# Optimization experiments

Measured on AMD Instinct MI355X. Metric: run time of the kernel, lower is better.

## Reference

```python
import jax, jax.numpy as jnp
import numpy as np

N_NODES = 100000
N_EDGES = 1600000
N_GRAPHS = 64
FEAT = 64
EMB = 64
HID = 64
VOCAB = 32


def setup_inputs() -> dict:
    key = jax.random.key(0)
    ks = jax.random.split(key, 20)
    w = lambda k, sh: (jax.random.normal(k, sh, jnp.float32) * 0.05)
    x = jax.random.normal(ks[0], (N_NODES, FEAT), jnp.float32)
    edge_index = jax.random.randint(ks[1], (2, N_EDGES), 0, N_NODES, dtype=jnp.int32).astype(jnp.int64)
    batch = jnp.sort(jax.random.randint(ks[2], (N_NODES,), 0, N_GRAPHS, dtype=jnp.int32)).astype(jnp.int64)
    return {
        'x': x, 'edge_index': edge_index, 'batch': batch,
        # RGCN layer 1 (single relation): relation weight, root weight, bias
        'W1': w(ks[3], (FEAT, EMB)), 'root1': w(ks[4], (FEAT, EMB)), 'b1': w(ks[5], (EMB,)),
        # RGCN layer 2
        'W2': w(ks[6], (EMB, HID)), 'root2': w(ks[7], (EMB, HID)), 'b2': w(ks[8], (HID,)),
        # init_h / init_c linear heads
        'Wh': w(ks[9], (HID, HID)), 'bh': w(ks[10], (HID,)),
        'Wc': w(ks[11], (HID, HID)), 'bc': w(ks[12], (HID,)),
        # output layer
        'Wo': w(ks[13], (HID, VOCAB)), 'bo': w(ks[14], (VOCAB,)),
    }


def _rgcn(x, edge_index, W, root, b):
    # PyG RGCNConv with num_relations=1, aggr='mean':
    # out[i] = mean_{j in N(i)} (x[j] @ W) + x[i] @ root + b
    src, dst = edge_index[0], edge_index[1]
    msg = x[src] @ W                                    # [E, out] gather + small GEMM
    agg = jax.ops.segment_sum(msg, dst, num_segments=x.shape[0])
    cnt = jax.ops.segment_sum(jnp.ones((edge_index.shape[1],), x.dtype), dst, num_segments=x.shape[0])
    agg = agg / jnp.maximum(cnt, 1.0)[:, None]
    return agg + x @ root + b


def reference(x, edge_index, batch, W1, root1, b1, W2, root2, b2, Wh, bh, Wc, bc, Wo, bo):
    h = jax.nn.relu(_rgcn(x, edge_index, W1, root1, b1))
    h = jax.nn.relu(_rgcn(h, edge_index, W2, root2, b2))
    # global_mean_pool over graph-assignment vector `batch`
    summ = jax.ops.segment_sum(h, batch, num_segments=N_GRAPHS)
    cnt = jax.ops.segment_sum(jnp.ones((h.shape[0],), h.dtype), batch, num_segments=N_GRAPHS)
    pooled = summ / jnp.maximum(cnt, 1.0)[:, None]      # [G, HID]
    hidden = pooled @ Wh + bh
    cell = pooled @ Wc + bc
    logits = jax.nn.log_softmax(hidden @ Wo + bo, axis=1)
    return (logits, hidden, cell)
```

## Files before the change

kernel.cpp:

```cpp
#include <hip/hip_runtime.h>
#include <hip/hip_bf16.h>


typedef __attribute__((ext_vector_type(8))) short short8;
typedef __attribute__((ext_vector_type(4))) float f32x4;
typedef __attribute__((ext_vector_type(2))) float f32x2;

#define RB 9
#define MAXBINS 256
#define CAP 12288
#define BCAP 14336
#define CHUNK 8192

__device__ inline float bf2f(unsigned short h) {
    return __uint_as_float(((unsigned int)h) << 16);
}
__device__ inline float bflo(unsigned int u) { return __uint_as_float(u << 16); }
__device__ inline float bfhi(unsigned int u) { return __uint_as_float(u & 0xffff0000u); }
__device__ inline unsigned short f2bf(float f) {
    unsigned int u = __float_as_uint(f);
    u = (u + 0x7fffu + ((u >> 16) & 1u)) >> 16;
    return (unsigned short)u;
}

__device__ inline void build_bfrag(const float* __restrict__ W,
                                   const float* __restrict__ R,
                                   int q, int mm, short8 bfrag[8][2]) {
#pragma unroll
    for (int t = 0; t < 8; ++t) {
        const int n = t * 16 + mm;
        const float* P = (n < 64) ? (W + n) : (R + n - 64);
#pragma unroll
        for (int c = 0; c < 2; ++c) {
#pragma unroll
            for (int j = 0; j < 8; ++j) {
                const int k = c * 32 + q * 8 + j;
                bfrag[t][c][j] = (short)f2bf(P[k * 64]);
            }
        }
    }
}

__device__ inline void store_xw_fp8(unsigned char* __restrict__ xw8, int rowbase, int q,
                                    int t, int mm, const f32x4& accT, int N) {
#pragma unroll
    for (int r = 0; r < 4; ++r) {
        const float v0 = accT[r];
        const float v1 = __shfl_down(v0, 1);
        const float v2 = __shfl_down(v0, 2);
        const float v3 = __shfl_down(v0, 3);
        const int orow = rowbase + q * 4 + r;
        if (!(mm & 3) && orow < N) {
            unsigned int u = (unsigned int)__builtin_amdgcn_cvt_pk_fp8_f32(v0, v1, 0, false);
            u = (unsigned int)__builtin_amdgcn_cvt_pk_fp8_f32(v2, v3, (int)u, true);
            *(unsigned int*)&xw8[(size_t)orow * 64 + t * 16 + mm] = u;
        }
    }
}

__global__ __launch_bounds__(256) void bin_gemm1(const int* __restrict__ src,
                                                 const int* __restrict__ dst,
                                                 unsigned int* __restrict__ coarse,
                                                 int* __restrict__ gcur,
                                                 int E, int BINS, int nbBin,
                                                 const float* __restrict__ x,
                                                 const float* __restrict__ W1,
                                                 const float* __restrict__ R1,
                                                 const float* __restrict__ bias,
                                                 unsigned char* __restrict__ xw8,
                                                 unsigned short* __restrict__ xrb,
                                                 int N) {
    __shared__ int cnt[MAXBINS];
    __shared__ int incl[MAXBINS];
    __shared__ int bstart[MAXBINS];
    __shared__ int bcur[MAXBINS];
    __shared__ int gbase[MAXBINS];
    __shared__ unsigned int stage[CHUNK];
    __shared__ unsigned char binOf[CHUNK];

    const int tid = threadIdx.x;
    if (blockIdx.x >= (unsigned)nbBin) {
        const int gb = blockIdx.x - nbBin;
        if (gb == 0 && tid < 16)
            *(unsigned int*)&xw8[(size_t)N * 64 + tid * 4] = 0u;

        const int lane = tid & 63;
        const int q = lane >> 4;
        const int mm = lane & 15;

        short8 bfrag[8][2];
        build_bfrag(W1, R1, q, mm, bfrag);
        float bv[4];
#pragma unroll
        for (int tt = 0; tt < 4; ++tt) bv[tt] = bias[tt * 16 + mm];

        const int wid = tid >> 6;
        const int gw = gb * 4 + wid;
        const int nw = 1024 * 4;
        const int ntiles = N >> 4;

        for (int tile = gw; tile < ntiles; tile += nw) {
            const int row0 = tile << 4;
            const float* ap = &x[(size_t)(row0 + mm) * 64 + q * 8];
            const float4 f0 = *(const float4*)ap;
            const float4 f1 = *(const float4*)(ap + 4);
            const float4 f2 = *(const float4*)(ap + 32);
            const float4 f3 = *(const float4*)(ap + 36);
            short8 a0, a1;
            a0[0] = (short)f2bf(f0.x); a0[1] = (short)f2bf(f0.y);
            a0[2] = (short)f2bf(f0.z); a0[3] = (short)f2bf(f0.w);
            a0[4] = (short)f2bf(f1.x); a0[5] = (short)f2bf(f1.y);
            a0[6] = (short)f2bf(f1.z); a0[7] = (short)f2bf(f1.w);
            a1[0] = (short)f2bf(f2.x); a1[1] = (short)f2bf(f2.y);
            a1[2] = (short)f2bf(f2.z); a1[3] = (short)f2bf(f2.w);
            a1[4] = (short)f2bf(f3.x); a1[5] = (short)f2bf(f3.y);
            a1[6] = (short)f2bf(f3.z); a1[7] = (short)f2bf(f3.w);
            f32x4 acc[8];
#pragma unroll
            for (int t = 0; t < 8; ++t) {
                acc[t] = (f32x4){0.f, 0.f, 0.f, 0.f};
                acc[t] = __builtin_amdgcn_mfma_f32_16x16x32_bf16(a0, bfrag[t][0], acc[t], 0, 0, 0);
                acc[t] = __builtin_amdgcn_mfma_f32_16x16x32_bf16(a1, bfrag[t][1], acc[t], 0, 0, 0);
            }
#pragma unroll
            for (int t = 0; t < 4; ++t) store_xw_fp8(xw8, row0, q, t, mm, acc[t], N);
#pragma unroll
            for (int t = 4; t < 8; ++t) {
#pragma unroll
                for (int r = 0; r < 4; ++r) {
                    const float v = acc[t][r] + bv[t - 4];
                    const float vn = __shfl_down(v, 1);
                    if (!(mm & 1)) {
                        const unsigned int u = (unsigned int)f2bf(v) | ((unsigned int)f2bf(vn) << 16);
                        *(unsigned int*)&xrb[(size_t)(row0 + q * 4 + r) * 64 + (t - 4) * 16 + mm] = u;
                    }
                }
            }
        }
        return;
    }

    const int chunk0 = blockIdx.x * CHUNK;
    int myS[32], myD[32];
#pragma unroll
    for (int k = 0; k < 32; ++k) {
        const int idx = chunk0 + k * 256 + tid;
        if (idx < E) { myS[k] = src[idx]; myD[k] = dst[idx]; }
        else myD[k] = -1;
    }
    cnt[tid] = 0;
    __syncthreads();
#pragma unroll
    for (int k = 0; k < 32; ++k)
        if (myD[k] >= 0) atomicAdd(&cnt[myD[k] >> RB], 1);
    __syncthreads();
    incl[tid] = cnt[tid];
    __syncthreads();
    for (int off = 1; off < 256; off <<= 1) {
        int t = (tid >= off) ? incl[tid - off] : 0;
        __syncthreads();
        incl[tid] += t;
        __syncthreads();
    }
    bstart[tid] = incl[tid] - cnt[tid];
    bcur[tid] = incl[tid] - cnt[tid];
    __syncthreads();
#pragma unroll
    for (int k = 0; k < 32; ++k) {
        if (myD[k] >= 0) {
            const int b = myD[k] >> RB;
            const int pos = atomicAdd(&bcur[b], 1);
            stage[pos] = (unsigned int)myS[k] | ((unsigned int)(myD[k] & ((1 << RB) - 1)) << 17);
            binOf[pos] = (unsigned char)b;
        }
    }
    __syncthreads();
    if (tid < BINS && cnt[tid] > 0)
        gbase[tid] = tid * CAP + atomicAdd(&gcur[tid], cnt[tid]);
    __syncthreads();
    int total = E - chunk0;
    if (total > CHUNK) total = CHUNK;
    for (int idx = tid; idx < total; idx += 256) {
        const int b = binOf[idx];
        coarse[gbase[b] + (idx - bstart[b])] = stage[idx];
    }
}

__global__ __launch_bounds__(256) void finalize_csr(const unsigned int* __restrict__ coarse,
                                                    const int* __restrict__ gcur,
                                                    int* __restrict__ bucket,
                                                    int* __restrict__ pstart,
                                                    int* __restrict__ degarr,
                                                    int N, int BINS) {
    __shared__ int ncnt[512];
    __shared__ int pexcl[512];
    __shared__ int ncur[512];
    __shared__ int s2[256];

    const int tid = threadIdx.x;
    const int b = blockIdx.x;
    const int cb = gcur[b];
    const int base = b * BCAP;
    const unsigned int* reg = coarse + (size_t)b * CAP;
    const int node0 = b << RB;
    int nloc = N - node0;
    if (nloc > 512) nloc = 512;

    ncnt[tid] = 0; ncnt[tid + 256] = 0;
    __syncthreads();
    for (int idx = tid; idx < cb; idx += 256)
        atomicAdd(&ncnt[reg[idx] >> 17], 1);
    __syncthreads();
    const int p0 = (ncnt[2 * tid] + 15) & ~15;
    const int p1 = (ncnt[2 * tid + 1] + 15) & ~15;
    s2[tid] = p0 + p1;
    __syncthreads();
    for (int off = 1; off < 256; off <<= 1) {
        int t = (tid >= off) ? s2[tid - off] : 0;
        __syncthreads();
        s2[tid] += t;
        __syncthreads();
    }
    const int pairExcl = s2[tid] - (p0 + p1);
    pexcl[2 * tid] = pairExcl;
    pexcl[2 * tid + 1] = pairExcl + p0;
    ncur[2 * tid] = pairExcl;
    ncur[2 * tid + 1] = pairExcl + p0;
    __syncthreads();
    for (int i = tid; i < nloc; i += 256) {
        pstart[node0 + i] = base + pexcl[i];
        degarr[node0 + i] = ncnt[i];
        const int dg = ncnt[i];
        const int pd = (dg + 15) & ~15;
        for (int j = dg; j < pd; ++j) bucket[base + pexcl[i] + j] = N;
    }
    for (int idx = tid; idx < cb; idx += 256) {
        const unsigned int e = reg[idx];
        const int p = atomicAdd(&ncur[e >> 17], 1);
        bucket[base + p] = (int)(e & 0x1FFFFu);
    }
}

__global__ __launch_bounds__(256) void aggregate(const unsigned char* __restrict__ xw8,
                                                 const unsigned short* __restrict__ xrb,
                                                 const int* __restrict__ pstart,
                                                 const int* __restrict__ degarr,
                                                 const int* __restrict__ bucket,
                                                 unsigned short* __restrict__ outb,
                                                 int N) {
    const int lane = threadIdx.x & 63;
    const int quarter = lane >> 4;
    const int fl = lane & 15;
    const int wid = threadIdx.x >> 6;
    const int gw = blockIdx.x * 4 + wid;
    const int nw = gridDim.x * 4;

    for (int i = gw; i < N; i += 4 * nw) {
        int idxs[4], r0[4], dg[4], pd[4];
#pragma unroll
        for (int j = 0; j < 4; ++j) {
            idxs[j] = i + j * nw;
            const bool hasJ = idxs[j] < N;
            const int ii = hasJ ? idxs[j] : i;
            r0[j] = pstart[ii];
            dg[j] = hasJ ? degarr[ii] : 0;
            pd[j] = (dg[j] + 15) & ~15;
        }
        int pdM = pd[0];
#pragma unroll
        for (int j = 1; j < 4; ++j) pdM = pd[j] > pdM ? pd[j] : pdM;

        float acc[4][4];
#pragma unroll
        for (int j = 0; j < 4; ++j)
#pragma unroll
            for (int c = 0; c < 4; ++c) acc[j][c] = 0.f;

        for (int base = 0; base < pdM; base += 64) {
            int s[4];
#pragma unroll
            for (int j = 0; j < 4; ++j) {
                const int rem = pd[j] - base;
                s[j] = (lane < rem) ? bucket[r0[j] + base + lane] : N;
            }
            int mx = pdM - base;
            if (mx > 64) mx = 64;
            for (int t = 0; t < mx; t += 16) {
                unsigned int u[4][4];
#pragma unroll
                for (int j = 0; j < 4; ++j)
#pragma unroll
                    for (int p = 0; p < 4; ++p) {
                        const int rr = __shfl(s[j], t + 4 * p + quarter);
                        u[j][p] = *(const unsigned int*)&xw8[(size_t)rr * 64 + fl * 4];
                    }
#pragma unroll
                for (int j = 0; j < 4; ++j)
#pragma unroll
                    for (int p = 0; p < 4; ++p) {
                        const f32x2 lo = __builtin_amdgcn_cvt_pk_f32_fp8(u[j][p], false);
                        const f32x2 hi = __builtin_amdgcn_cvt_pk_f32_fp8(u[j][p], true);
                        acc[j][0] += lo.x; acc[j][1] += lo.y;
                        acc[j][2] += hi.x; acc[j][3] += hi.y;
                    }
            }
        }
#pragma unroll
        for (int j = 0; j < 4; ++j)
#pragma unroll
            for (int c = 0; c < 4; ++c) {
                acc[j][c] += __shfl_xor(acc[j][c], 16);
                acc[j][c] += __shfl_xor(acc[j][c], 32);
            }

        if (quarter == 0) {
#pragma unroll
            for (int j = 0; j < 4; ++j) {
                if (idxs[j] < N) {
                    const float inv = 1.0f / (float)(dg[j] > 0 ? dg[j] : 1);
                    const uint2 ur = *(const uint2*)&xrb[(size_t)idxs[j] * 64 + fl * 4];
                    const float o0 = fmaxf(acc[j][0] * inv + bflo(ur.x), 0.f);
                    const float o1 = fmaxf(acc[j][1] * inv + bfhi(ur.x), 0.f);
                    const float o2 = fmaxf(acc[j][2] * inv + bflo(ur.y), 0.f);
                    const float o3 = fmaxf(acc[j][3] * inv + bfhi(ur.y), 0.f);
                    uint2 w;
                    w.x = (unsigned int)f2bf(o0) | ((unsigned int)f2bf(o1) << 16);
                    w.y = (unsigned int)f2bf(o2) | ((unsigned int)f2bf(o3) << 16);
                    *(uint2*)&outb[(size_t)idxs[j] * 64 + fl * 4] = w;
                }
            }
        }
    }
}

__global__ __launch_bounds__(256) void gemm_xwr2(const unsigned short* __restrict__ xin,
                                                 const float* __restrict__ W2,
                                                 const float* __restrict__ R2,
                                                 const float* __restrict__ bias,
                                                 unsigned char* __restrict__ xw8,
                                                 unsigned short* __restrict__ xrb,
                                                 int M) {
    if (blockIdx.x == 0 && threadIdx.x < 16)
        *(unsigned int*)&xw8[(size_t)M * 64 + threadIdx.x * 4] = 0u;

    const int lane = threadIdx.x & 63;
    const int q = lane >> 4;
    const int mm = lane & 15;

    short8 bfrag[8][2];
    build_bfrag(W2, R2, q, mm, bfrag);
    float bv[4];
#pragma unroll
    for (int tt = 0; tt < 4; ++tt) bv[tt] = bias[tt * 16 + mm];

    const int wid = threadIdx.x >> 6;
    const int gw = blockIdx.x * 4 + wid;
    const int nw = gridDim.x * 4;
    const int ntiles = M >> 4;

    for (int tile = gw; tile < ntiles; tile += nw) {
        const int row0 = tile << 4;
        const short8 a0 = *(const short8*)&xin[(size_t)(row0 + mm) * 64 + q * 8];
        const short8 a1 = *(const short8*)&xin[(size_t)(row0 + mm) * 64 + 32 + q * 8];
        f32x4 acc[8];
#pragma unroll
        for (int t = 0; t < 8; ++t) {
            acc[t] = (f32x4){0.f, 0.f, 0.f, 0.f};
            acc[t] = __builtin_amdgcn_mfma_f32_16x16x32_bf16(a0, bfrag[t][0], acc[t], 0, 0, 0);
            acc[t] = __builtin_amdgcn_mfma_f32_16x16x32_bf16(a1, bfrag[t][1], acc[t], 0, 0, 0);
        }
#pragma unroll
        for (int t = 0; t < 4; ++t) store_xw_fp8(xw8, row0, q, t, mm, acc[t], M);
#pragma unroll
        for (int t = 4; t < 8; ++t) {
#pragma unroll
            for (int r = 0; r < 4; ++r) {
                const float v = acc[t][r] + bv[t - 4];
                const float vn = __shfl_down(v, 1);
                if (!(mm & 1)) {
                    const unsigned int u = (unsigned int)f2bf(v) | ((unsigned int)f2bf(vn) << 16);
                    *(unsigned int*)&xrb[(size_t)(row0 + q * 4 + r) * 64 + (t - 4) * 16 + mm] = u;
                }
            }
        }
    }
}

__global__ __launch_bounds__(256) void pool_kernel(const unsigned short* __restrict__ h,
                                                   const int* __restrict__ batch,
                                                   float* __restrict__ gsum, int N) {
    __shared__ float red[16][64];
    __shared__ int bnds[2];
    const int gph = blockIdx.x >> 2;
    const int part = blockIdx.x & 3;
    if (threadIdx.x < 2) {
        const int target = gph + threadIdx.x;
        int lo = 0, hi = N;
        while (lo < hi) {
            int mid = (lo + hi) >> 1;
            if (batch[mid] < target) lo = mid + 1; else hi = mid;
        }
        bnds[threadIdx.x] = lo;
    }
    __syncthreads();
    const int r0 = bnds[0], tot = bnds[1] - bnds[0];
    const int pr0 = r0 + (tot * part) / 4;
    const int pr1 = r0 + (tot * (part + 1)) / 4;
    const int f = threadIdx.x & 15;
    const int r = threadIdx.x >> 4;
    float4 acc = {0.f, 0.f, 0.f, 0.f};
    for (int row = pr0 + r; row < pr1; row += 16) {
        const ushort4 v = *(const ushort4*)&h[(size_t)row * 64 + f * 4];
        acc.x += bf2f(v.x); acc.y += bf2f(v.y);
        acc.z += bf2f(v.z); acc.w += bf2f(v.w);
    }
    red[r][f * 4 + 0] = acc.x; red[r][f * 4 + 1] = acc.y;
    red[r][f * 4 + 2] = acc.z; red[r][f * 4 + 3] = acc.w;
    __syncthreads();
    if (threadIdx.x < 64) {
        float s = 0.f;
        for (int j = 0; j < 16; ++j) s += red[j][threadIdx.x];
        atomicAdd(&gsum[gph * 64 + threadIdx.x], s);
    }
}

__global__ __launch_bounds__(256) void head_kernel(const float* __restrict__ gsum,
                                                   const int* __restrict__ batch,
                                                   const float* __restrict__ Wh,
                                                   const float* __restrict__ bh,
                                                   const float* __restrict__ Wc,
                                                   const float* __restrict__ bc,
                                                   const float* __restrict__ Wo,
                                                   const float* __restrict__ bo,
                                                   float* __restrict__ out, int N) {
    __shared__ float pm[4096];
    __shared__ float Ws[4096];
    __shared__ float Cs[4096];
    __shared__ float hid[4096];
    __shared__ int bnds[65];
    const int t = threadIdx.x;

    if (t < 65) {
        int lo = 0, hi = N;
        while (lo < hi) {
            int mid = (lo + hi) >> 1;
            if (batch[mid] < t) lo = mid + 1; else hi = mid;
        }
        bnds[t] = lo;
    }
    __syncthreads();
    for (int idx = t; idx < 1024; idx += 256) {
        const int g = idx >> 4;
        const int c = bnds[g + 1] - bnds[g];
        const float inv = 1.0f / (float)(c > 0 ? c : 1);
        float4 v = ((const float4*)gsum)[idx];
        v.x *= inv; v.y *= inv; v.z *= inv; v.w *= inv;
        ((float4*)pm)[idx] = v;
        ((float4*)Ws)[idx] = ((const float4*)Wh)[idx];
        ((float4*)Cs)[idx] = ((const float4*)Wc)[idx];
    }
    __syncthreads();

    const int w = t >> 6;
    const int l = t & 63;
    const float bhv = bh[l], bcv = bc[l];
    float ah[16], ac[16];
#pragma unroll
    for (int i = 0; i < 16; ++i) { ah[i] = bhv; ac[i] = bcv; }
    const float* pmw = pm + ((w << 4) << 6);
#pragma unroll 4
    for (int k = 0; k < 64; ++k) {
        const float wv = Ws[(k << 6) + l];
        const float cv = Cs[(k << 6) + l];
#pragma unroll
        for (int i = 0; i < 16; ++i) {
            const float p = pmw[(i << 6) + k];
            ah[i] = fmaf(p, wv, ah[i]);
            ac[i] = fmaf(p, cv, ac[i]);
        }
    }
#pragma unroll
    for (int i = 0; i < 16; ++i) {
        const int g = (w << 4) + i;
        hid[(g << 6) + l] = ah[i];
        out[2048 + (g << 6) + l] = ah[i];
        out[6144 + (g << 6) + l] = ac[i];
    }
    __syncthreads();
    for (int idx = t; idx < 512; idx += 256)
        ((float4*)Ws)[idx] = ((const float4*)Wo)[idx];
    __syncthreads();

    const int v = l & 31;
    const int gh = l >> 5;
    const int g0 = ((w << 1) + gh) << 3;
    const float bov = bo[v];
    float lgacc[8];
#pragma unroll
    for (int i = 0; i < 8; ++i) lgacc[i] = bov;
#pragma unroll 4
    for (int k = 0; k < 64; ++k) {
        const float wv = Ws[(k << 5) + v];
#pragma unroll
        for (int i = 0; i < 8; ++i)
            lgacc[i] = fmaf(hid[((g0 + i) << 6) + k], wv, lgacc[i]);
    }
    float* lg = pm;
#pragma unroll
    for (int i = 0; i < 8; ++i) lg[((g0 + i) << 5) + v] = lgacc[i];
    __syncthreads();

    const int g = t >> 2;
    const int vs = (t & 3) << 3;
    const float* row = lg + (g << 5);
    float mx = -3.4e38f;
#pragma unroll
    for (int j = 0; j < 8; ++j) mx = fmaxf(mx, row[vs + j]);
    mx = fmaxf(mx, __shfl_xor(mx, 1));
    mx = fmaxf(mx, __shfl_xor(mx, 2));
    float s = 0.f;
#pragma unroll
    for (int j = 0; j < 8; ++j) s += __expf(row[vs + j] - mx);
    s += __shfl_xor(s, 1);
    s += __shfl_xor(s, 2);
    const float lse = mx + __logf(s);
#pragma unroll
    for (int j = 0; j < 8; ++j) out[(g << 5) + vs + j] = row[vs + j] - lse;
}

extern "C" void kernel_launch(void* const* d_in, const int* in_sizes, int n_in,
                              void* d_out, int out_size, void* d_ws, size_t ws_size,
                              hipStream_t stream) {
    const float* x = (const float*)d_in[0];
    const int* ei = (const int*)d_in[1];
    const int* batch = (const int*)d_in[2];
    const float* W1 = (const float*)d_in[3];
    const float* root1 = (const float*)d_in[4];
    const float* b1 = (const float*)d_in[5];
    const float* W2 = (const float*)d_in[6];
    const float* root2 = (const float*)d_in[7];
    const float* b2 = (const float*)d_in[8];
    const float* Wh = (const float*)d_in[9];
    const float* bh = (const float*)d_in[10];
    const float* Wc = (const float*)d_in[11];
    const float* bc = (const float*)d_in[12];
    const float* Wo = (const float*)d_in[13];
    const float* bo = (const float*)d_in[14];
    float* out = (float*)d_out;

    const int N = in_sizes[0] / 64;
    const int E = in_sizes[1] / 2;
    const int* srcp = ei;
    const int* dstp = ei + E;
    const int BINS = (N + (1 << RB) - 1) >> RB;

    char* ws = (char*)d_ws;
    size_t off = 0;
    auto alloc = [&](size_t bytes) -> void* {
        void* p = ws + off;
        off += (bytes + 255) & ~(size_t)255;
        return p;
    };
    int* pstart = (int*)alloc((size_t)N * 4);
    int* degarr = (int*)alloc((size_t)N * 4);
    int* bucket = (int*)alloc(((size_t)BINS * BCAP + 256) * 4);
    unsigned int* coarse = (unsigned int*)alloc((size_t)BINS * CAP * 4);
    unsigned short* h1 = (unsigned short*)alloc((size_t)N * 64 * 2);
    unsigned short* h2 = (unsigned short*)alloc((size_t)N * 64 * 2);
    unsigned char* xw8 = (unsigned char*)alloc((size_t)(N + 1) * 64);
    unsigned char* xw8b = (unsigned char*)alloc((size_t)(N + 1) * 64);
    unsigned short* xrb = (unsigned short*)alloc((size_t)N * 64 * 2);
    unsigned short* xrb2 = (unsigned short*)alloc((size_t)N * 64 * 2);
    int* gcur = (int*)alloc(MAXBINS * 4);
    float* gsum = (float*)alloc(4096 * 4);

    const int nbBin = (E + CHUNK - 1) / CHUNK;

    hipMemsetAsync(gcur, 0, MAXBINS * 4 + 4096 * 4, stream);
    bin_gemm1<<<nbBin + 1024, 256, 0, stream>>>(srcp, dstp, coarse, gcur, E, BINS, nbBin,
                                                x, W1, root1, b1, xw8, xrb, N);
    finalize_csr<<<BINS, 256, 0, stream>>>(coarse, gcur, bucket, pstart, degarr, N, BINS);
    aggregate<<<4096, 256, 0, stream>>>(xw8, xrb, pstart, degarr, bucket, h1, N);
    gemm_xwr2<<<1024, 256, 0, stream>>>(h1, W2, root2, b2, xw8b, xrb2, N);
    aggregate<<<4096, 256, 0, stream>>>(xw8b, xrb2, pstart, degarr, bucket, h2, N);
    pool_kernel<<<256, 256, 0, stream>>>(h2, batch, gsum, N);
    head_kernel<<<1, 256, 0, stream>>>(gsum, batch, Wh, bh, Wc, bc, Wo, bo, out, N);
}
```

Baseline: 275.6 us.

## Halve binning chunk, drop pad writes, skip padded gathers, resize aggregate grid

The edge-binning chunk is halved to 4096 edges per block. The CSR finalize no longer writes sentinel padding entries; instead aggregate loads bucket entries only up to the true degree and skips 16-edge gather groups beyond each node's own padded degree. It also accumulates with packed f32x2 adds, prefetches the root rows early, uses 32-bit address math, and launches one wave per node group (N/16 blocks). Together these aim to cut wasted gathers, redundant writes and loop overhead. Skipped pad slots rely on the s=N sentinel pointing at the zeroed row at index N.

```diff
diff --git a/kernel.cpp b/kernel.cpp
--- a/kernel.cpp
+++ b/kernel.cpp
@@ -10,7 +10,7 @@
 #define MAXBINS 256
 #define CAP 12288
 #define BCAP 14336
-#define CHUNK 8192
+#define CHUNK 4096
 
 __device__ inline float bf2f(unsigned short h) {
     return __uint_as_float(((unsigned int)h) << 16);
@@ -141,9 +141,9 @@
     }
 
     const int chunk0 = blockIdx.x * CHUNK;
-    int myS[32], myD[32];
-#pragma unroll
-    for (int k = 0; k < 32; ++k) {
+    int myS[16], myD[16];
+#pragma unroll
+    for (int k = 0; k < 16; ++k) {
         const int idx = chunk0 + k * 256 + tid;
         if (idx < E) { myS[k] = src[idx]; myD[k] = dst[idx]; }
         else myD[k] = -1;
@@ -151,7 +151,7 @@
     cnt[tid] = 0;
     __syncthreads();
 #pragma unroll
-    for (int k = 0; k < 32; ++k)
+    for (int k = 0; k < 16; ++k)
         if (myD[k] >= 0) atomicAdd(&cnt[myD[k] >> RB], 1);
     __syncthreads();
     incl[tid] = cnt[tid];
@@ -166,7 +166,7 @@
     bcur[tid] = incl[tid] - cnt[tid];
     __syncthreads();
 #pragma unroll
-    for (int k = 0; k < 32; ++k) {
+    for (int k = 0; k < 16; ++k) {
         if (myD[k] >= 0) {
             const int b = myD[k] >> RB;
             const int pos = atomicAdd(&bcur[b], 1);
@@ -230,9 +230,6 @@
     for (int i = tid; i < nloc; i += 256) {
         pstart[node0 + i] = base + pexcl[i];
         degarr[node0 + i] = ncnt[i];
-        const int dg = ncnt[i];
-        const int pd = (dg + 15) & ~15;
-        for (int j = dg; j < pd; ++j) bucket[base + pexcl[i] + j] = N;
     }
     for (int idx = tid; idx < cb; idx += 256) {
         const unsigned int e = reg[idx];
@@ -254,6 +251,7 @@
     const int wid = threadIdx.x >> 6;
     const int gw = blockIdx.x * 4 + wid;
     const int nw = gridDim.x * 4;
+    const unsigned flo = (unsigned)(fl << 2);
 
     for (int i = gw; i < N; i += 4 * nw) {
         int idxs[4], r0[4], dg[4], pd[4];
@@ -270,64 +268,77 @@
 #pragma unroll
         for (int j = 1; j < 4; ++j) pdM = pd[j] > pdM ? pd[j] : pdM;
 
-        float acc[4][4];
-#pragma unroll
-        for (int j = 0; j < 4; ++j)
-#pragma unroll
-            for (int c = 0; c < 4; ++c) acc[j][c] = 0.f;
+        uint2 ur[4];
+#pragma unroll
+        for (int j = 0; j < 4; ++j) { ur[j].x = 0u; ur[j].y = 0u; }
+        if (quarter == 0) {
+#pragma unroll
+            for (int j = 0; j < 4; ++j)
+                if (idxs[j] < N)
+                    ur[j] = *(const uint2*)&xrb[(size_t)idxs[j] * 64 + fl * 4];
+        }
+
+        f32x2 alo[4], ahi[4];
+#pragma unroll
+        for (int j = 0; j < 4; ++j) {
+            alo[j] = (f32x2){0.f, 0.f};
+            ahi[j] = (f32x2){0.f, 0.f};
+        }
 
         for (int base = 0; base < pdM; base += 64) {
-            int s[4];
+            int s[4], mxj[4];
 #pragma unroll
             for (int j = 0; j < 4; ++j) {
+                const int trm = dg[j] - base;
+                s[j] = N;
+                if (trm > 0 && lane < trm)
+                    s[j] = *(const int*)((const char*)bucket + ((unsigned)(r0[j] + base + lane) << 2));
                 const int rem = pd[j] - base;
-                s[j] = (lane < rem) ? bucket[r0[j] + base + lane] : N;
+                mxj[j] = rem < 64 ? rem : 64;
             }
             int mx = pdM - base;
             if (mx > 64) mx = 64;
             for (int t = 0; t < mx; t += 16) {
                 unsigned int u[4][4];
 #pragma unroll
-                for (int j = 0; j < 4; ++j)
-#pragma unroll
-                    for (int p = 0; p < 4; ++p) {
-                        const int rr = __shfl(s[j], t + 4 * p + quarter);
-                        u[j][p] = *(const unsigned int*)&xw8[(size_t)rr * 64 + fl * 4];
+                for (int j = 0; j < 4; ++j) {
+                    if (t < mxj[j]) {
+#pragma unroll
+                        for (int p = 0; p < 4; ++p) {
+                            const unsigned rr = (unsigned)__shfl(s[j], t + 4 * p + quarter);
+                            u[j][p] = *(const unsigned int*)(xw8 + ((rr << 6) | flo));
+                        }
                     }
-#pragma unroll
-                for (int j = 0; j < 4; ++j)
-#pragma unroll
-                    for (int p = 0; p < 4; ++p) {
-                        const f32x2 lo = __builtin_amdgcn_cvt_pk_f32_fp8(u[j][p], false);
-                        const f32x2 hi = __builtin_amdgcn_cvt_pk_f32_fp8(u[j][p], true);
-                        acc[j][0] += lo.x; acc[j][1] += lo.y;
-                        acc[j][2] += hi.x; acc[j][3] += hi.y;
+                }
+#pragma unroll
+                for (int j = 0; j < 4; ++j) {
+                    if (t < mxj[j]) {
+#pragma unroll
+                        for (int p = 0; p < 4; ++p) {
+                            alo[j] += __builtin_amdgcn_cvt_pk_f32_fp8(u[j][p], false);
+                            ahi[j] += __builtin_amdgcn_cvt_pk_f32_fp8(u[j][p], true);
+                        }
                     }
+                }
             }
         }
 #pragma unroll
-        for (int j = 0; j < 4; ++j)
-#pragma unroll
-            for (int c = 0; c < 4; ++c) {
-                acc[j][c] += __shfl_xor(acc[j][c], 16);
-                acc[j][c] += __shfl_xor(acc[j][c], 32);
-            }
-
-        if (quarter == 0) {
-#pragma unroll
-            for (int j = 0; j < 4; ++j) {
-                if (idxs[j] < N) {
-                    const float inv = 1.0f / (float)(dg[j] > 0 ? dg[j] : 1);
-                    const uint2 ur = *(const uint2*)&xrb[(size_t)idxs[j] * 64 + fl * 4];
-                    const float o0 = fmaxf(acc[j][0] * inv + bflo(ur.x), 0.f);
-                    const float o1 = fmaxf(acc[j][1] * inv + bfhi(ur.x), 0.f);
-                    const float o2 = fmaxf(acc[j][2] * inv + bflo(ur.y), 0.f);
-                    const float o3 = fmaxf(acc[j][3] * inv + bfhi(ur.y), 0.f);
-                    uint2 w;
-                    w.x = (unsigned int)f2bf(o0) | ((unsigned int)f2bf(o1) << 16);
-                    w.y = (unsigned int)f2bf(o2) | ((unsigned int)f2bf(o3) << 16);
-                    *(uint2*)&outb[(size_t)idxs[j] * 64 + fl * 4] = w;
-                }
+        for (int j = 0; j < 4; ++j) {
+            float a0 = alo[j].x, a1 = alo[j].y, a2 = ahi[j].x, a3 = ahi[j].y;
+            a0 += __shfl_xor(a0, 16); a1 += __shfl_xor(a1, 16);
+            a2 += __shfl_xor(a2, 16); a3 += __shfl_xor(a3, 16);
+            a0 += __shfl_xor(a0, 32); a1 += __shfl_xor(a1, 32);
+            a2 += __shfl_xor(a2, 32); a3 += __shfl_xor(a3, 32);
+            if (quarter == 0 && idxs[j] < N) {
+                const float inv = 1.0f / (float)(dg[j] > 0 ? dg[j] : 1);
+                const float o0 = fmaxf(a0 * inv + bflo(ur[j].x), 0.f);
+                const float o1 = fmaxf(a1 * inv + bfhi(ur[j].x), 0.f);
+                const float o2 = fmaxf(a2 * inv + bflo(ur[j].y), 0.f);
+                const float o3 = fmaxf(a3 * inv + bfhi(ur[j].y), 0.f);
+                uint2 w;
+                w.x = (unsigned int)f2bf(o0) | ((unsigned int)f2bf(o1) << 16);
+                w.y = (unsigned int)f2bf(o2) | ((unsigned int)f2bf(o3) << 16);
+                *(uint2*)&outb[(size_t)idxs[j] * 64 + fl * 4] = w;
             }
         }
     }
@@ -575,14 +586,15 @@
     float* gsum = (float*)alloc(4096 * 4);
 
     const int nbBin = (E + CHUNK - 1) / CHUNK;
+    const int aggBlocks = (N + 15) / 16;
 
     hipMemsetAsync(gcur, 0, MAXBINS * 4 + 4096 * 4, stream);
     bin_gemm1<<<nbBin + 1024, 256, 0, stream>>>(srcp, dstp, coarse, gcur, E, BINS, nbBin,
                                                 x, W1, root1, b1, xw8, xrb, N);
     finalize_csr<<<BINS, 256, 0, stream>>>(coarse, gcur, bucket, pstart, degarr, N, BINS);
-    aggregate<<<4096, 256, 0, stream>>>(xw8, xrb, pstart, degarr, bucket, h1, N);
+    aggregate<<<aggBlocks, 256, 0, stream>>>(xw8, xrb, pstart, degarr, bucket, h1, N);
     gemm_xwr2<<<1024, 256, 0, stream>>>(h1, W2, root2, b2, xw8b, xrb2, N);
-    aggregate<<<4096, 256, 0, stream>>>(xw8b, xrb2, pstart, degarr, bucket, h2, N);
+    aggregate<<<aggBlocks, 256, 0, stream>>>(xw8b, xrb2, pstart, degarr, bucket, h2, N);
     pool_kernel<<<256, 256, 0, stream>>>(h2, batch, gsum, N);
     head_kernel<<<1, 256, 0, stream>>>(gsum, batch, Wh, bh, Wc, bc, Wo, bo, out, N);
 }
```

Result: faster. 259.9 us (-5.7%).
